# Optimization experiments

Hardware: AMD Instinct MI355X
Metric: run time of the kernel (lower is better)

## Reference

```python
import jax, jax.numpy as jnp
import numpy as np


def setup_inputs() -> dict:
    key = jax.random.key(0)
    k1, k2, k3 = jax.random.split(key, 3)
    B, C_IN, C_OUT, K, S = 2, 16, 16, 3, 24
    x = jax.random.normal(k1, (B, C_IN, S, S, S, S), dtype=jnp.float32)
    # weight in canonical [out, in, kh, kw, kd, kt] layout (the torch module's
    # pre-permutation is a storage detail; the math is a standard 4D cross-correlation)
    w = jax.random.normal(k2, (C_OUT, C_IN, K, K, K, K), dtype=jnp.float32) * 0.05
    b = jax.random.normal(k3, (C_OUT,), dtype=jnp.float32) * 0.05
    return {"x": x, "w": w, "b": b}


def reference(x, w, b):
    # 4D convolution with 'same' padding (pad = k//2 in every spatial dim),
    # stride 1, no dilation — exactly what the looped conv4d() computes.
    dn = jax.lax.conv_dimension_numbers(x.shape, w.shape, ("NCHWDT", "OIHWDT", "NCHWDT"))
    out = jax.lax.conv_general_dilated(
        x, w,
        window_strides=(1, 1, 1, 1),
        padding="SAME",
        dimension_numbers=dn,
    )
    return out + b[None, :, None, None, None, None]
```

## Files before the change

kernel.cpp:

```cpp
#include <hip/hip_runtime.h>

typedef __attribute__((ext_vector_type(8))) short bfrag;
typedef __attribute__((ext_vector_type(4))) float f32x4;

#define XS4 331776
#define XS3 13824
#define XS2 576

#define WS_ZERO   86016
#define WS_XS     86080
#define XS_HALF_B 5308416
#define WS_NEED   42553408ull
#define NSITE     1260
#define NSITE_PAD 1280
#define LDS_LO    20480

__global__ void presplit_kernel(const float* __restrict__ x,
                                const float* __restrict__ w,
                                unsigned int* __restrict__ ws,
                                unsigned short* __restrict__ xs) {
    int bid = blockIdx.x;
    int tid = threadIdx.x;
    if (bid < 84) {
        int e = bid * 256 + tid;
        int ci2 = e & 3;
        int co  = (e >> 2) & 15;
        int t84 = e >> 6;
        int tau = t84 % 84;
        int cs  = t84 / 84;
        int ch  = cs >> 1;
        int s   = cs & 1;
        unsigned int outv = 0u;
        if (tau < 81) {
            unsigned int half[2];
#pragma unroll
            for (int q = 0; q < 2; ++q) {
                int ci = ch * 8 + ci2 * 2 + q;
                union { float f; unsigned u; } v;
                v.f = w[(co * 16 + ci) * 81 + tau];
                unsigned hi = v.u & 0xFFFF0000u;
                union { unsigned u; float f; } hv; hv.u = hi;
                union { float f; unsigned u; } rv; rv.f = v.f - hv.f;
                unsigned lo = rv.u & 0xFFFF0000u;
                half[q] = (s == 0) ? hi : lo;
            }
            outv = (half[0] >> 16) | (half[1] & 0xFFFF0000u);
        }
        ws[e] = outv;
        if (e < 16) ws[(WS_ZERO / 4) + e] = 0u;
    } else {
        int xb = bid - 84;
        int s4 = (xb % 1296) * 256 + tid;
        int bc = xb / 1296;
        const float* xp = x + (size_t)(bc * 8) * XS4 + s4;
        unsigned hib[8], lob[8];
#pragma unroll
        for (int c = 0; c < 8; ++c) {
            union { float f; unsigned u; } v;
            v.f = xp[(size_t)c * XS4];
            unsigned hi = v.u & 0xFFFF0000u;
            union { unsigned u; float f; } hv; hv.u = hi;
            union { float f; unsigned u; } rv; rv.f = v.f - hv.f;
            hib[c] = hi;
            lob[c] = rv.u & 0xFFFF0000u;
        }
        uint4 ph, pl;
        ph.x = (hib[0] >> 16) | (hib[1] & 0xFFFF0000u);
        ph.y = (hib[2] >> 16) | (hib[3] & 0xFFFF0000u);
        ph.z = (hib[4] >> 16) | (hib[5] & 0xFFFF0000u);
        ph.w = (hib[6] >> 16) | (hib[7] & 0xFFFF0000u);
        pl.x = (lob[0] >> 16) | (lob[1] & 0xFFFF0000u);
        pl.y = (lob[2] >> 16) | (lob[3] & 0xFFFF0000u);
        pl.z = (lob[4] >> 16) | (lob[5] & 0xFFFF0000u);
        pl.w = (lob[6] >> 16) | (lob[7] & 0xFFFF0000u);
        *(uint4*)(xs + ((size_t)(bc * 2 + 0) * XS4 + s4) * 8) = ph;
        *(uint4*)(xs + ((size_t)(bc * 2 + 1) * XS4 + s4) * 8) = pl;
    }
}

__global__ __launch_bounds__(192, 3)
void conv4d_mfma_v3(const unsigned short* __restrict__ xs,
                    const unsigned short* __restrict__ wfrag,
                    const char* __restrict__ zptr,
                    const float* __restrict__ bias,
                    float* __restrict__ out) {
    __shared__ __align__(16) unsigned short xhl[2 * NSITE_PAD * 8];

    const int tid  = threadIdx.x;
    const int l    = tid & 63;
    const int wv   = tid >> 6;

    int bid = blockIdx.x;
    const int b    = bid / 3456;
    int r          = bid % 3456;
    const int h    = r / 144;
    r              = r % 144;
    const int w0   = r / 6;
    const int seg  = r % 6;
    const int dbase = (seg >> 1) * 8, tbase = (seg & 1) * 12;

    const int i_  = l & 15;
    const int tl4 = l >> 4;
    const int d_i = i_ >> 2;
    const int t_i = i_ & 3;
    const int co  = l & 15;

    const int mt0 = wv * 2, mt1 = wv * 2 + 1;
    const int dq0 = mt0 / 3, tq0 = mt0 % 3;
    const int dq1 = mt1 / 3, tq1 = mt1 % 3;
    const int la0 = tq0 * 640 + t_i * 160 + dq0 * 64 + d_i * 16;
    const int la1 = tq1 * 640 + t_i * 160 + dq1 * 64 + d_i * 16;

    int aoffs[21];
#pragma unroll
    for (int g = 0; g < 21; ++g) {
        int tau  = 4 * g + tl4;
        int teff = tau > 80 ? 80 : tau;
        int p    = teff / 9;
        int r9   = teff - p * 9;
        int kd   = r9 / 3;
        int kt   = r9 - kd * 3;
        aoffs[g] = p * 2240 + kt * 160 + kd * 16;
    }

    f32x4 acc0 = {0.f, 0.f, 0.f, 0.f};
    f32x4 acc1 = {0.f, 0.f, 0.f, 0.f};

    const char* xbase = (const char*)&xhl[0];
    const char* xsb   = (const char*)xs;
    const char* wB    = (const char*)wfrag + tl4 * 256 + co * 16;

    for (int ch = 0; ch < 2; ++ch) {
        __syncthreads();

        const unsigned base16 = (unsigned)((b * 2 + ch) * 2) * (unsigned)(XS4 * 16);

        for (int k = 0; k < 7; ++k) {
            int idx0 = k * 192 + wv * 64;
            if (idx0 < NSITE_PAD) {
                int idx = idx0 + l;
                int p  = idx / 140;
                int rr = idx - p * 140;
                int tt = rr / 10;
                int dd = rr - tt * 10;
                int hh = h  + p / 3 - 1;
                int ww = w0 + p % 3 - 1;
                int dp = dbase + dd - 1;
                int tp = tbase + tt - 1;
                bool valid = ((unsigned)hh < 24u) && ((unsigned)ww < 24u) &&
                             ((unsigned)dp < 24u) && ((unsigned)tp < 24u) &&
                             (idx < NSITE);
                const char* gh = zptr;
                const char* gl = zptr;
                if (valid) {
                    unsigned off = base16 +
                        (unsigned)(hh * XS3 + ww * XS2 + dp * 24 + tp) * 16u;
                    gh = xsb + off;
                    gl = gh + XS_HALF_B;
                }
                char* lp = (char*)&xhl[0] + idx * 16;
                __builtin_amdgcn_global_load_lds(
                    (const __attribute__((address_space(1))) void*)gh,
                    (__attribute__((address_space(3))) void*)lp, 16, 0, 0);
                __builtin_amdgcn_global_load_lds(
                    (const __attribute__((address_space(1))) void*)gl,
                    (__attribute__((address_space(3))) void*)(lp + LDS_LO), 16, 0, 0);
            }
        }
        __syncthreads();

        const char* pw = wB + ch * 43008;

#pragma unroll
        for (int g = 0; g < 21; ++g) {
            bfrag whf = *(const bfrag*)(pw + g * 1024);
            bfrag wlf = *(const bfrag*)(pw + g * 1024 + 21504);

            const char* ax = xbase + aoffs[g];
            bfrag xh0 = *(const bfrag*)(ax + la0);
            bfrag xl0 = *(const bfrag*)(ax + la0 + LDS_LO);
            bfrag xh1 = *(const bfrag*)(ax + la1);
            bfrag xl1 = *(const bfrag*)(ax + la1 + LDS_LO);

            __builtin_amdgcn_s_setprio(1);
            acc0 = __builtin_amdgcn_mfma_f32_16x16x32_bf16(xh0, whf, acc0, 0, 0, 0);
            acc1 = __builtin_amdgcn_mfma_f32_16x16x32_bf16(xh1, whf, acc1, 0, 0, 0);
            acc0 = __builtin_amdgcn_mfma_f32_16x16x32_bf16(xh0, wlf, acc0, 0, 0, 0);
            acc1 = __builtin_amdgcn_mfma_f32_16x16x32_bf16(xh1, wlf, acc1, 0, 0, 0);
            acc0 = __builtin_amdgcn_mfma_f32_16x16x32_bf16(xl0, whf, acc0, 0, 0, 0);
            acc1 = __builtin_amdgcn_mfma_f32_16x16x32_bf16(xl1, whf, acc1, 0, 0, 0);
            __builtin_amdgcn_s_setprio(0);
        }
    }

    const float bv = bias[co];
    const int ob = (b * 16 + co) * XS4 + h * XS3 + w0 * XS2;
    {
        int d = dbase + dq0 * 4 + tl4;
        int t = tbase + tq0 * 4;
        float4 v;
        v.x = acc0[0] + bv; v.y = acc0[1] + bv;
        v.z = acc0[2] + bv; v.w = acc0[3] + bv;
        *(float4*)&out[ob + d * 24 + t] = v;
    }
    {
        int d = dbase + dq1 * 4 + tl4;
        int t = tbase + tq1 * 4;
        float4 v;
        v.x = acc1[0] + bv; v.y = acc1[1] + bv;
        v.z = acc1[2] + bv; v.w = acc1[3] + bv;
        *(float4*)&out[ob + d * 24 + t] = v;
    }
}

__global__ void wsplit_kernel(const float* __restrict__ w,
                              unsigned int* __restrict__ ws) {
    int e = blockIdx.x * 256 + threadIdx.x;
    int ci2 = e & 3;
    int co  = (e >> 2) & 15;
    int t84 = e >> 6;
    int tau = t84 % 84;
    int cs  = t84 / 84;
    int ch  = cs >> 1;
    int s   = cs & 1;
    unsigned int outv = 0u;
    if (tau < 81) {
        unsigned int half[2];
#pragma unroll
        for (int q = 0; q < 2; ++q) {
            int ci = ch * 8 + ci2 * 2 + q;
            union { float f; unsigned u; } v;
            v.f = w[(co * 16 + ci) * 81 + tau];
            unsigned hi = v.u & 0xFFFF0000u;
            union { unsigned u; float f; } hv; hv.u = hi;
            union { float f; unsigned u; } rv; rv.f = v.f - hv.f;
            unsigned lo = rv.u & 0xFFFF0000u;
            half[q] = (s == 0) ? hi : lo;
        }
        outv = (half[0] >> 16) | (half[1] & 0xFFFF0000u);
    }
    ws[e] = outv;
}

__global__ __launch_bounds__(192, 3)
void conv4d_mfma_v1(const float* __restrict__ x,
                    const unsigned short* __restrict__ wfrag,
                    const float* __restrict__ bias,
                    float* __restrict__ out) {
    __shared__ __align__(16) unsigned short xhl[2][1260][8];

    const int tid = threadIdx.x;
    const int l   = tid & 63;

    int bid = blockIdx.x;
    const int b    = bid / 3456;
    int r          = bid % 3456;
    const int h    = r / 144;
    r              = r % 144;
    const int w0   = r / 6;
    const int seg  = r % 6;
    const int dbase = (seg >> 1) * 8, tbase = (seg & 1) * 12;

    const int i_  = l & 15;
    const int tl4 = l >> 4;
    const int d_i = i_ >> 2;
    const int t_i = i_ & 3;
    const int co  = l & 15;

    const int wv  = tid >> 6;
    const int mt0 = wv * 2, mt1 = wv * 2 + 1;
    const int dq0 = mt0 / 3, tq0 = mt0 % 3;
    const int dq1 = mt1 / 3, tq1 = mt1 % 3;
    const int la0 = dq0 * 896 + tq0 * 64 + d_i * 224 + t_i * 16;
    const int la1 = dq1 * 896 + tq1 * 64 + d_i * 224 + t_i * 16;

    f32x4 acc0 = {0.f, 0.f, 0.f, 0.f};
    f32x4 acc1 = {0.f, 0.f, 0.f, 0.f};

    const char* xbase = (const char*)&xhl[0][0][0];
    const char* wB    = (const char*)wfrag + tl4 * 256 + co * 16;

    for (int ch = 0; ch < 2; ++ch) {
        __syncthreads();
        for (int k = 0; k < 7; ++k) {
            int idx = tid + k * 192;
            if (idx < 1260) {
                int p  = idx / 140;
                int rr = idx - p * 140;
                int dd = rr / 14;
                int tt = rr - dd * 14;
                int hh = h  + p / 3 - 1;
                int ww = w0 + p % 3 - 1;
                int dp = dbase + dd - 1;
                int tp = tbase + tt - 1;
                unsigned hib[8], lob[8];
                bool valid = ((unsigned)hh < 24u) && ((unsigned)ww < 24u) &&
                             ((unsigned)dp < 24u) && ((unsigned)tp < 24u);
                if (valid) {
                    int g = b * (16 * XS4) + (ch * 8) * XS4
                          + hh * XS3 + ww * XS2 + dp * 24 + tp;
#pragma unroll
                    for (int c = 0; c < 8; ++c) {
                        union { float f; unsigned u; } v;
                        v.f = x[g + c * XS4];
                        unsigned hi = v.u & 0xFFFF0000u;
                        union { unsigned u; float f; } hv; hv.u = hi;
                        union { float f; unsigned u; } rv2; rv2.f = v.f - hv.f;
                        hib[c] = hi;
                        lob[c] = rv2.u & 0xFFFF0000u;
                    }
                } else {
#pragma unroll
                    for (int c = 0; c < 8; ++c) { hib[c] = 0u; lob[c] = 0u; }
                }
                uint4 ph, pl;
                ph.x = (hib[0] >> 16) | (hib[1] & 0xFFFF0000u);
                ph.y = (hib[2] >> 16) | (hib[3] & 0xFFFF0000u);
                ph.z = (hib[4] >> 16) | (hib[5] & 0xFFFF0000u);
                ph.w = (hib[6] >> 16) | (hib[7] & 0xFFFF0000u);
                pl.x = (lob[0] >> 16) | (lob[1] & 0xFFFF0000u);
                pl.y = (lob[2] >> 16) | (lob[3] & 0xFFFF0000u);
                pl.z = (lob[4] >> 16) | (lob[5] & 0xFFFF0000u);
                pl.w = (lob[6] >> 16) | (lob[7] & 0xFFFF0000u);
                *(uint4*)((char*)&xhl[0][0][0] + idx * 16)         = ph;
                *(uint4*)((char*)&xhl[0][0][0] + 20160 + idx * 16) = pl;
            }
        }
        __syncthreads();

        const char* pw = wB + ch * 43008;
#pragma unroll
        for (int g = 0; g < 21; ++g) {
            bfrag whf = *(const bfrag*)(pw + g * 1024);
            bfrag wlf = *(const bfrag*)(pw + g * 1024 + 21504);

            int tau  = 4 * g + tl4;
            int teff = tau > 80 ? 80 : tau;
            int p    = teff / 9;
            int r9   = teff - p * 9;
            int kd   = r9 / 3;
            int kt   = r9 - kd * 3;
            int aoff = p * 2240 + kd * 224 + kt * 16;

            const char* ax = xbase + aoff;
            bfrag xh0 = *(const bfrag*)(ax + la0);
            bfrag xl0 = *(const bfrag*)(ax + la0 + 20160);
            bfrag xh1 = *(const bfrag*)(ax + la1);
            bfrag xl1 = *(const bfrag*)(ax + la1 + 20160);

            acc0 = __builtin_amdgcn_mfma_f32_16x16x32_bf16(xh0, whf, acc0, 0, 0, 0);
            acc1 = __builtin_amdgcn_mfma_f32_16x16x32_bf16(xh1, whf, acc1, 0, 0, 0);
            acc0 = __builtin_amdgcn_mfma_f32_16x16x32_bf16(xh0, wlf, acc0, 0, 0, 0);
            acc1 = __builtin_amdgcn_mfma_f32_16x16x32_bf16(xh1, wlf, acc1, 0, 0, 0);
            acc0 = __builtin_amdgcn_mfma_f32_16x16x32_bf16(xl0, whf, acc0, 0, 0, 0);
            acc1 = __builtin_amdgcn_mfma_f32_16x16x32_bf16(xl1, whf, acc1, 0, 0, 0);
        }
    }

    const float bv = bias[co];
    const int ob = (b * 16 + co) * XS4 + h * XS3 + w0 * XS2;
    {
        int d = dbase + dq0 * 4 + tl4;
        int t = tbase + tq0 * 4;
        float4 v;
        v.x = acc0[0] + bv; v.y = acc0[1] + bv;
        v.z = acc0[2] + bv; v.w = acc0[3] + bv;
        *(float4*)&out[ob + d * 24 + t] = v;
    }
    {
        int d = dbase + dq1 * 4 + tl4;
        int t = tbase + tq1 * 4;
        float4 v;
        v.x = acc1[0] + bv; v.y = acc1[1] + bv;
        v.z = acc1[2] + bv; v.w = acc1[3] + bv;
        *(float4*)&out[ob + d * 24 + t] = v;
    }
}

extern "C" void kernel_launch(void* const* d_in, const int* in_sizes, int n_in,
                              void* d_out, int out_size, void* d_ws, size_t ws_size,
                              hipStream_t stream) {
    const float* x    = (const float*)d_in[0];
    const float* w    = (const float*)d_in[1];
    const float* bias = (const float*)d_in[2];
    float* out        = (float*)d_out;
    char* ws          = (char*)d_ws;
    unsigned* wfrag   = (unsigned*)ws;

    if (ws_size >= WS_NEED) {
        unsigned short* xsq = (unsigned short*)(ws + WS_XS);
        presplit_kernel<<<84 + 5184, 256, 0, stream>>>(x, w, wfrag, xsq);
        conv4d_mfma_v3<<<6912, 192, 0, stream>>>(
            xsq, (const unsigned short*)wfrag, ws + WS_ZERO, bias, out);
    } else {
        wsplit_kernel<<<84, 256, 0, stream>>>(w, wfrag);
        conv4d_mfma_v1<<<6912, 192, 0, stream>>>(
            x, (const unsigned short*)wfrag, bias, out);
    }
}
```

Baseline: 238.8 us.

## Double-buffer input halos across four stages with larger per-block tiles

Replaces the v3 conv kernel with a pipelined version. Each block now covers a full t-row (24 outputs) with 4 waves, each holding 3 accumulators. The input halo is streamed in four stages (channel half × hi/lo split) into two LDS buffers, so the next stage's global-to-LDS loads overlap the MFMAs on the current stage. The lo-input pass now pairs only with the hi weights, matching the previous three-product split. Block IDs are also remapped to spread neighbours across XCDs. This is meant to hide load latency and improve halo reuse, at the cost of larger LDS use and lower occupancy.

Result: faster. 228.0 us (-4.6%).

```diff
diff --git a/kernel.cpp b/kernel.cpp
--- a/kernel.cpp
+++ b/kernel.cpp
@@ -11,9 +11,8 @@
 #define WS_XS     86080
 #define XS_HALF_B 5308416
 #define WS_NEED   42553408ull
-#define NSITE     1260
-#define NSITE_PAD 1280
-#define LDS_LO    20480
+#define NSITE2    2340
+#define NPAD2     2560
 
 __global__ void presplit_kernel(const float* __restrict__ x,
                                 const float* __restrict__ w,
@@ -78,26 +77,27 @@
     }
 }
 
-__global__ __launch_bounds__(192, 3)
-void conv4d_mfma_v3(const unsigned short* __restrict__ xs,
-                    const unsigned short* __restrict__ wfrag,
-                    const char* __restrict__ zptr,
-                    const float* __restrict__ bias,
-                    float* __restrict__ out) {
-    __shared__ __align__(16) unsigned short xhl[2 * NSITE_PAD * 8];
-
-    const int tid  = threadIdx.x;
-    const int l    = tid & 63;
-    const int wv   = tid >> 6;
-
-    int bid = blockIdx.x;
-    const int b    = bid / 3456;
-    int r          = bid % 3456;
-    const int h    = r / 144;
-    r              = r % 144;
-    const int w0   = r / 6;
-    const int seg  = r % 6;
-    const int dbase = (seg >> 1) * 8, tbase = (seg & 1) * 12;
+__global__ __launch_bounds__(256, 2)
+void conv4d_pipe(const unsigned short* __restrict__ xs,
+                 const unsigned short* __restrict__ wfrag,
+                 const char* __restrict__ zptr,
+                 const float* __restrict__ bias,
+                 float* __restrict__ out) {
+    __shared__ __align__(16) unsigned short xbuf[2][NPAD2 * 8];
+
+    const int tid = threadIdx.x;
+    const int l   = tid & 63;
+    const int wv  = tid >> 6;
+
+    int bid0 = blockIdx.x;
+    int bid  = (bid0 & 7) * 432 + (bid0 >> 3);
+    const int b    = bid / 1728;
+    int r          = bid % 1728;
+    const int h    = r / 72;  r %= 72;
+    const int w0   = r / 3;
+    const int dseg = r % 3;
+    const int dbase = dseg * 8;
+    const int b4   = b * 4;
 
     const int i_  = l & 15;
     const int tl4 = l >> 4;
@@ -105,13 +105,41 @@
     const int t_i = i_ & 3;
     const int co  = l & 15;
 
-    const int mt0 = wv * 2, mt1 = wv * 2 + 1;
-    const int dq0 = mt0 / 3, tq0 = mt0 % 3;
-    const int dq1 = mt1 / 3, tq1 = mt1 % 3;
-    const int la0 = tq0 * 640 + t_i * 160 + dq0 * 64 + d_i * 16;
-    const int la1 = tq1 * 640 + t_i * 160 + dq1 * 64 + d_i * 16;
-
-    int aoffs[21];
+    int voff[10];
+#pragma unroll
+    for (int it = 0; it < 10; ++it) {
+        int idx = it * 256 + tid;
+        int p  = idx / 260;
+        int rr = idx - p * 260;
+        int tt = rr / 10;
+        int dd = rr - tt * 10;
+        int hh = h  + p / 3 - 1;
+        int ww = w0 + p % 3 - 1;
+        int dp = dbase + dd - 1;
+        int tp = tt - 1;
+        bool valid = ((unsigned)hh < 24u) && ((unsigned)ww < 24u) &&
+                     ((unsigned)dp < 24u) && ((unsigned)tp < 24u) &&
+                     (idx < NSITE2);
+        voff[it] = valid ? (hh * XS3 + ww * XS2 + dp * 24 + tp) * 16 : -1;
+    }
+
+    const char* xsb = (const char*)xs;
+
+#define STAGE(K, PB) {                                                         \
+    const char* gb = xsb + (size_t)(b4 + (K)) * (size_t)(XS4 * 16);            \
+    char* lb = (char*)&xbuf[(PB)][0];                                          \
+    _Pragma("unroll")                                                          \
+    for (int it = 0; it < 10; ++it) {                                          \
+        const char* g = (voff[it] >= 0) ? (gb + voff[it]) : zptr;              \
+        __builtin_amdgcn_global_load_lds(                                      \
+            (const __attribute__((address_space(1))) void*)g,                  \
+            (__attribute__((address_space(3))) void*)(lb + (it * 256 + tid) * 16), \
+            16, 0, 0);                                                         \
+    } }
+
+    STAGE(0, 0);
+
+    int goff[21];
 #pragma unroll
     for (int g = 0; g < 21; ++g) {
         int tau  = 4 * g + tl4;
@@ -120,95 +148,77 @@
         int r9   = teff - p * 9;
         int kd   = r9 / 3;
         int kt   = r9 - kd * 3;
-        aoffs[g] = p * 2240 + kt * 160 + kd * 16;
-    }
-
-    f32x4 acc0 = {0.f, 0.f, 0.f, 0.f};
-    f32x4 acc1 = {0.f, 0.f, 0.f, 0.f};
-
-    const char* xbase = (const char*)&xhl[0];
-    const char* xsb   = (const char*)xs;
-    const char* wB    = (const char*)wfrag + tl4 * 256 + co * 16;
-
-    for (int ch = 0; ch < 2; ++ch) {
+        goff[g]  = p * 4160 + kt * 160 + kd * 16;
+    }
+    int la[3];
+#pragma unroll
+    for (int j = 0; j < 3; ++j) {
+        int mt = wv * 3 + j;
+        int dq = mt / 6, tq = mt % 6;
+        la[j] = (tq * 4 + t_i) * 160 + (dq * 4 + d_i) * 16;
+    }
+
+    f32x4 acc[3];
+#pragma unroll
+    for (int j = 0; j < 3; ++j) acc[j] = (f32x4){0.f, 0.f, 0.f, 0.f};
+
+    const char* wB = (const char*)wfrag + tl4 * 256 + co * 16;
+
+#pragma unroll
+    for (int k = 0; k < 4; ++k) {
         __syncthreads();
-
-        const unsigned base16 = (unsigned)((b * 2 + ch) * 2) * (unsigned)(XS4 * 16);
-
-        for (int k = 0; k < 7; ++k) {
-            int idx0 = k * 192 + wv * 64;
-            if (idx0 < NSITE_PAD) {
-                int idx = idx0 + l;
-                int p  = idx / 140;
-                int rr = idx - p * 140;
-                int tt = rr / 10;
-                int dd = rr - tt * 10;
-                int hh = h  + p / 3 - 1;
-                int ww = w0 + p % 3 - 1;
-                int dp = dbase + dd - 1;
-                int tp = tbase + tt - 1;
-                bool valid = ((unsigned)hh < 24u) && ((unsigned)ww < 24u) &&
-                             ((unsigned)dp < 24u) && ((unsigned)tp < 24u) &&
-                             (idx < NSITE);
-                const char* gh = zptr;
-                const char* gl = zptr;
-                if (valid) {
-                    unsigned off = base16 +
-                        (unsigned)(hh * XS3 + ww * XS2 + dp * 24 + tp) * 16u;
-                    gh = xsb + off;
-                    gl = gh + XS_HALF_B;
-                }
-                char* lp = (char*)&xhl[0] + idx * 16;
-                __builtin_amdgcn_global_load_lds(
-                    (const __attribute__((address_space(1))) void*)gh,
-                    (__attribute__((address_space(3))) void*)lp, 16, 0, 0);
-                __builtin_amdgcn_global_load_lds(
-                    (const __attribute__((address_space(1))) void*)gl,
-                    (__attribute__((address_space(3))) void*)(lp + LDS_LO), 16, 0, 0);
+        if (k < 3) STAGE(k + 1, (k + 1) & 1);
+
+        const char* pw = wB + (k >> 1) * 43008;
+        const char* sb = (const char*)&xbuf[k & 1][0];
+
+        if ((k & 1) == 0) {
+#pragma unroll
+            for (int g = 0; g < 21; ++g) {
+                bfrag wh = *(const bfrag*)(pw + g * 1024);
+                bfrag wl = *(const bfrag*)(pw + g * 1024 + 21504);
+                const char* ax = sb + goff[g];
+                bfrag x0 = *(const bfrag*)(ax + la[0]);
+                bfrag x1 = *(const bfrag*)(ax + la[1]);
+                bfrag x2 = *(const bfrag*)(ax + la[2]);
+                __builtin_amdgcn_s_setprio(1);
+                acc[0] = __builtin_amdgcn_mfma_f32_16x16x32_bf16(x0, wh, acc[0], 0, 0, 0);
+                acc[1] = __builtin_amdgcn_mfma_f32_16x16x32_bf16(x1, wh, acc[1], 0, 0, 0);
+                acc[2] = __builtin_amdgcn_mfma_f32_16x16x32_bf16(x2, wh, acc[2], 0, 0, 0);
+                acc[0] = __builtin_amdgcn_mfma_f32_16x16x32_bf16(x0, wl, acc[0], 0, 0, 0);
+                acc[1] = __builtin_amdgcn_mfma_f32_16x16x32_bf16(x1, wl, acc[1], 0, 0, 0);
+                acc[2] = __builtin_amdgcn_mfma_f32_16x16x32_bf16(x2, wl, acc[2], 0, 0, 0);
+                __builtin_amdgcn_s_setprio(0);
             }
-        }
-        __syncthreads();
-
-        const char* pw = wB + ch * 43008;
-
-#pragma unroll
-        for (int g = 0; g < 21; ++g) {
-            bfrag whf = *(const bfrag*)(pw + g * 1024);
-            bfrag wlf = *(const bfrag*)(pw + g * 1024 + 21504);
-
-            const char* ax = xbase + aoffs[g];
-            bfrag xh0 = *(const bfrag*)(ax + la0);
-            bfrag xl0 = *(const bfrag*)(ax + la0 + LDS_LO);
-            bfrag xh1 = *(const bfrag*)(ax + la1);
-            bfrag xl1 = *(const bfrag*)(ax + la1 + LDS_LO);
-
-            __builtin_amdgcn_s_setprio(1);
-            acc0 = __builtin_amdgcn_mfma_f32_16x16x32_bf16(xh0, whf, acc0, 0, 0, 0);
-            acc1 = __builtin_amdgcn_mfma_f32_16x16x32_bf16(xh1, whf, acc1, 0, 0, 0);
-            acc0 = __builtin_amdgcn_mfma_f32_16x16x32_bf16(xh0, wlf, acc0, 0, 0, 0);
-            acc1 = __builtin_amdgcn_mfma_f32_16x16x32_bf16(xh1, wlf, acc1, 0, 0, 0);
-            acc0 = __builtin_amdgcn_mfma_f32_16x16x32_bf16(xl0, whf, acc0, 0, 0, 0);
-            acc1 = __builtin_amdgcn_mfma_f32_16x16x32_bf16(xl1, whf, acc1, 0, 0, 0);
-            __builtin_amdgcn_s_setprio(0);
-        }
-    }
+        } else {
+#pragma unroll
+            for (int g = 0; g < 21; ++g) {
+                bfrag wh = *(const bfrag*)(pw + g * 1024);
+                const char* ax = sb + goff[g];
+                bfrag x0 = *(const bfrag*)(ax + la[0]);
+                bfrag x1 = *(const bfrag*)(ax + la[1]);
+                bfrag x2 = *(const bfrag*)(ax + la[2]);
+                __builtin_amdgcn_s_setprio(1);
+                acc[0] = __builtin_amdgcn_mfma_f32_16x16x32_bf16(x0, wh, acc[0], 0, 0, 0);
+                acc[1] = __builtin_amdgcn_mfma_f32_16x16x32_bf16(x1, wh, acc[1], 0, 0, 0);
+                acc[2] = __builtin_amdgcn_mfma_f32_16x16x32_bf16(x2, wh, acc[2], 0, 0, 0);
+                __builtin_amdgcn_s_setprio(0);
+            }
+        }
+    }
+#undef STAGE
 
     const float bv = bias[co];
-    const int ob = (b * 16 + co) * XS4 + h * XS3 + w0 * XS2;
-    {
-        int d = dbase + dq0 * 4 + tl4;
-        int t = tbase + tq0 * 4;
+    const size_t ob = (size_t)(b * 16 + co) * XS4 + h * XS3 + w0 * XS2;
+#pragma unroll
+    for (int j = 0; j < 3; ++j) {
+        int mt = wv * 3 + j;
+        int dq = mt / 6, tq = mt % 6;
+        int d = dbase + dq * 4 + tl4;
+        int t = tq * 4;
         float4 v;
-        v.x = acc0[0] + bv; v.y = acc0[1] + bv;
-        v.z = acc0[2] + bv; v.w = acc0[3] + bv;
-        *(float4*)&out[ob + d * 24 + t] = v;
-    }
-    {
-        int d = dbase + dq1 * 4 + tl4;
-        int t = tbase + tq1 * 4;
-        float4 v;
-        v.x = acc1[0] + bv; v.y = acc1[1] + bv;
-        v.z = acc1[2] + bv; v.w = acc1[3] + bv;
+        v.x = acc[j][0] + bv; v.y = acc[j][1] + bv;
+        v.z = acc[j][2] + bv; v.w = acc[j][3] + bv;
         *(float4*)&out[ob + d * 24 + t] = v;
     }
 }
@@ -390,7 +400,7 @@
     if (ws_size >= WS_NEED) {
         unsigned short* xsq = (unsigned short*)(ws + WS_XS);
         presplit_kernel<<<84 + 5184, 256, 0, stream>>>(x, w, wfrag, xsq);
-        conv4d_mfma_v3<<<6912, 192, 0, stream>>>(
+        conv4d_pipe<<<3456, 256, 0, stream>>>(
             xsq, (const unsigned short*)wfrag, ws + WS_ZERO, bias, out);
     } else {
         wsplit_kernel<<<84, 256, 0, stream>>>(w, wfrag);
```
